# Kernel tuning notes

Measured on AMD Instinct MI355X. Metric: run time of the kernel, lower is better.

## Reference

```python
import jax, jax.numpy as jnp
import numpy as np


def _get_mask(in_features, out_features, in_flow_features, mask_type=None):
    # Faithful port of the torch get_mask() used by MADE.
    if mask_type == 'input':
        in_degrees = np.arange(in_features) % in_flow_features
    else:
        in_degrees = np.arange(in_features) % (in_flow_features - 1)
    if mask_type == 'output':
        out_degrees = np.arange(out_features) % in_flow_features - 1
    else:
        out_degrees = np.arange(out_features) % (in_flow_features - 1)
    return jnp.asarray((out_degrees[:, None] >= in_degrees[None, :]).astype(np.float32))


def setup_inputs() -> dict:
    B, D, H = 8192, 128, 2048
    key = jax.random.key(0)
    ks = jax.random.split(key, 7)
    w_scale_in = 1.0 / np.sqrt(D)
    w_scale_h = 1.0 / np.sqrt(H)
    return {
        'inputs': jax.random.normal(ks[0], (B, D), dtype=jnp.float32),
        's_w0': jax.random.normal(ks[1], (H, D), dtype=jnp.float32) * w_scale_in,
        's_b0': jnp.zeros((H,), dtype=jnp.float32),
        's_w1': jax.random.normal(ks[2], (H, H), dtype=jnp.float32) * w_scale_h,
        's_b1': jnp.zeros((H,), dtype=jnp.float32),
        's_w2': jax.random.normal(ks[3], (D, H), dtype=jnp.float32) * w_scale_h,
        's_b2': jnp.zeros((D,), dtype=jnp.float32),
        't_w0': jax.random.normal(ks[4], (H, D), dtype=jnp.float32) * w_scale_in,
        't_b0': jnp.zeros((H,), dtype=jnp.float32),
        't_w1': jax.random.normal(ks[5], (H, H), dtype=jnp.float32) * w_scale_h,
        't_b1': jnp.zeros((H,), dtype=jnp.float32),
        't_w2': jax.random.normal(ks[6], (D, H), dtype=jnp.float32) * w_scale_h,
        't_b2': jnp.zeros((D,), dtype=jnp.float32),
    }


def reference(inputs, s_w0, s_b0, s_w1, s_b1, s_w2, s_b2,
              t_w0, t_b0, t_w1, t_b1, t_w2, t_b2):
    # MADESplit forward, mode='direct', num_cond_inputs=None, pre_exp_tanh=False.
    D = inputs.shape[1]
    H = s_w0.shape[0]
    m_in = _get_mask(D, H, D, 'input')    # [H, D]
    m_h = _get_mask(H, H, D)              # [H, H]
    m_out = _get_mask(H, D, D, 'output')  # [D, H]

    def masked_mlp(w0, b0, w1, b1, w2, b2, act):
        h = act(inputs @ (m_in * w0).T + b0)   # joiner + first trunk activation
        h = act(h @ (m_h * w1).T + b1)
        return h @ (m_out * w2).T + b2

    m = masked_mlp(s_w0, s_b0, s_w1, s_b1, s_w2, s_b2, jnp.tanh)
    a = masked_mlp(t_w0, t_b0, t_w1, t_b1, t_w2, t_b2, jax.nn.relu)
    u = (inputs - m) * jnp.exp(-a)
    return u, -a.sum(-1, keepdims=True)
```

## Files before the change

kernel.cpp:

```cpp
#include <hip/hip_runtime.h>
#include <hip/hip_bf16.h>

typedef unsigned short u16;
typedef __attribute__((ext_vector_type(8))) short bf16x8;
typedef __attribute__((ext_vector_type(4))) float f32x4;

constexpr int NB = 8192, ND = 128, NH = 2048;

__device__ __forceinline__ u16 f2bf(float x) {
  union { float f; unsigned u; } v; v.f = x;
  unsigned r = v.u + 0x7fffu + ((v.u >> 16) & 1u);
  return (u16)(r >> 16);
}
__device__ __forceinline__ float bf2f(u16 h) {
  union { unsigned u; float f; } v; v.u = ((unsigned)h) << 16; return v.f;
}
__device__ __forceinline__ void store_split(u16* hi, u16* lo, long i, float v) {
  u16 h = f2bf(v);
  hi[i] = h;
  lo[i] = f2bf(v - bf2f(h));
}

__device__ __forceinline__ int deg_sorted(int j) {
  return (j < 272) ? (j / 17) : ((j - 16) >> 4);
}
__device__ __forceinline__ int perm_h(int j) {
  int g, r;
  if (j < 272) { g = j / 17; r = j - g * 17; }
  else         { g = (j - 16) >> 4; r = (j - 16) & 15; }
  return g + 127 * r;
}
__device__ __forceinline__ int offset_of_deg(int g) {
  return (g < 16) ? 17 * g : 16 * g + 16;
}

__device__ __forceinline__ void gll16(const u16* g, u16* l) {
  __builtin_amdgcn_global_load_lds(
      (const __attribute__((address_space(1))) unsigned*)g,
      (__attribute__((address_space(3))) unsigned*)l, 16, 0, 0);
}

__device__ __forceinline__ f32x4 mfma_bb(bf16x8 a, bf16x8 b, f32x4 c) {
  return __builtin_amdgcn_mfma_f32_16x16x32_bf16(a, b, c, 0, 0, 0);
}

template <int PHASE>
__global__ void prep_small(const float* __restrict__ x,
                           const float* __restrict__ w0,
                           const float* __restrict__ b0, const float* __restrict__ b1,
                           u16* __restrict__ xhi, u16* __restrict__ xlo,
                           u16* __restrict__ w0hi, u16* __restrict__ w0lo,
                           float* __restrict__ b0p, float* __restrict__ b1p) {
  constexpr int XB  = (NB * ND) / 256;
  constexpr int W0B = (NH * ND) / 256;
  int bid = blockIdx.x;
  const int tid = threadIdx.x;

  if (PHASE == 0) {
    if (bid < XB) {
      long i = (long)bid * 256 + tid;
      store_split(xhi, xlo, i, x[i]);
      return;
    }
    bid -= XB;
  }
  if (bid < W0B) {
    int i = bid * 256 + tid;
    int r_out = i >> 7, c = i & 127;
    float v = (deg_sorted(r_out) >= c) ? w0[perm_h(r_out) * ND + c] : 0.0f;
    store_split(w0hi, w0lo, i, v);
    return;
  }
  bid -= W0B;
  if (bid < 8) { int j = bid * 256 + tid; b0p[j] = b0[perm_h(j)]; return; }
  { int j = (bid - 8) * 256 + tid; b1p[j] = b1[perm_h(j)]; }
}

__global__ void prep_rows(const float* __restrict__ w1, const float* __restrict__ w2,
                          u16* __restrict__ w1hi, u16* __restrict__ w1lo,
                          u16* __restrict__ w2hi, u16* __restrict__ w2lo) {
  __shared__ float row[NH];
  const int j = blockIdx.x;
  const int tid = threadIdx.x;
  const float* src = (j < NH) ? (w1 + (long)perm_h(j) * NH)
                              : (w2 + (long)(j - NH) * NH);
  const float4* s4 = (const float4*)src;
  float4* r4 = (float4*)row;
#pragma unroll
  for (int i = 0; i < 2; ++i) r4[tid + i * 256] = s4[tid + i * 256];
  __syncthreads();
  if (j < NH) {
    const int dj = deg_sorted(j);
    const long base = (long)j * NH;
#pragma unroll
    for (int k = 0; k < 8; ++k) {
      int c = k * 256 + tid;
      float v = (dj >= deg_sorted(c)) ? row[perm_h(c)] : 0.0f;
      store_split(w1hi, w1lo, base + c, v);
    }
  } else {
    const int r = j - NH;
    const long base = (long)r * NH;
#pragma unroll
    for (int k = 0; k < 8; ++k) {
      int c = k * 256 + tid;
      float v = ((r - 1) >= deg_sorted(c)) ? row[perm_h(c)] : 0.0f;
      store_split(w2hi, w2lo, base + c, v);
    }
  }
}

template <int ACT, int BOUND>
__global__ __launch_bounds__(256, 3) void gemm_split(
    const u16* __restrict__ Ahi, const u16* __restrict__ Alo,
    const u16* __restrict__ Bhi, const u16* __restrict__ Blo,
    const float* __restrict__ bias,
    u16* __restrict__ Chi, u16* __restrict__ Clo,
    float* __restrict__ Cf,
    int M, int N, int K, int ksteps_arg) {
  const int tid = threadIdx.x;
  const int l = tid & 63;
  const int w = tid >> 6;
  const int wr = w >> 1, wc = w & 1;
  const int bm = blockIdx.y * 128;
  const int NT = gridDim.x;
  const int bx = blockIdx.x;
  const int ntile = (bx & 1) ? (bx >> 1) : (NT - 1 - (bx >> 1));
  const int bn = ntile * 128;
  int ksteps;
  if (BOUND == 1) {
    int ghi = deg_sorted(bn + 127);
    ksteps = (ghi + 1 + 31) >> 5;
  } else if (BOUND == 2) {
    int ghi = deg_sorted(bn + 127);
    ksteps = (offset_of_deg(ghi + 1) + 31) >> 5;
  } else {
    ksteps = ksteps_arg;
  }
  const long kbase = (long)blockIdx.z * ksteps * 32;

  __shared__ __align__(16) u16 sAhi[4096];
  __shared__ __align__(16) u16 sAlo[4096];
  __shared__ __align__(16) u16 sBhi[4096];
  __shared__ __align__(16) u16 sBlo[4096];

  f32x4 acc[4][4] = {};

  const int srow = tid >> 2;
  const int scol = (tid & 3) << 3;
  const long aOff0 = (long)(bm + srow) * K + scol + kbase;
  const long aOff1 = aOff0 + 64L * K;
  const long bOff0 = (long)(bn + srow) * K + scol + kbase;
  const long bOff1 = bOff0 + 64L * K;
  const int ldst0 = tid * 8;
  const int ldst1 = 2048 + tid * 8;

  const int fr = l & 15, fq = l >> 4;

  for (int ks = 0; ks < ksteps; ++ks) {
    const long kk = (long)ks * 32;
    __syncthreads();
    gll16(Ahi + aOff0 + kk, sAhi + ldst0);
    gll16(Ahi + aOff1 + kk, sAhi + ldst1);
    gll16(Alo + aOff0 + kk, sAlo + ldst0);
    gll16(Alo + aOff1 + kk, sAlo + ldst1);
    gll16(Bhi + bOff0 + kk, sBhi + ldst0);
    gll16(Bhi + bOff1 + kk, sBhi + ldst1);
    gll16(Blo + bOff0 + kk, sBlo + ldst0);
    gll16(Blo + bOff1 + kk, sBlo + ldst1);
    __syncthreads();

    bf16x8 ah[4], alo[4], bh[4], blo[4];
#pragma unroll
    for (int m = 0; m < 4; ++m) {
      const int off = (wr * 64 + m * 16 + fr) * 32 + fq * 8;
      ah[m]  = *(const bf16x8*)(sAhi + off);
      alo[m] = *(const bf16x8*)(sAlo + off);
    }
#pragma unroll
    for (int n = 0; n < 4; ++n) {
      const int off = (wc * 64 + n * 16 + fr) * 32 + fq * 8;
      bh[n]  = *(const bf16x8*)(sBhi + off);
      blo[n] = *(const bf16x8*)(sBlo + off);
    }
#pragma unroll
    for (int m = 0; m < 4; ++m)
#pragma unroll
      for (int n = 0; n < 4; ++n) {
        acc[m][n] = mfma_bb(ah[m],  bh[n],  acc[m][n]);
        acc[m][n] = mfma_bb(alo[m], bh[n],  acc[m][n]);
        acc[m][n] = mfma_bb(ah[m],  blo[n], acc[m][n]);
      }
  }

  if (ACT == 2) {
    float* out = Cf + (long)blockIdx.z * M * N;
#pragma unroll
    for (int m = 0; m < 4; ++m) {
      const int row = bm + wr * 64 + m * 16 + fq * 4;
#pragma unroll
      for (int n = 0; n < 4; ++n) {
        const int col = bn + wc * 64 + n * 16 + fr;
#pragma unroll
        for (int r = 0; r < 4; ++r)
          out[(long)(row + r) * N + col] = acc[m][n][r];
      }
    }
  } else {
#pragma unroll
    for (int m = 0; m < 4; ++m) {
      const int row = bm + wr * 64 + m * 16 + fq * 4;
#pragma unroll
      for (int n = 0; n < 4; ++n) {
        const int col = bn + wc * 64 + n * 16 + fr;
        const float bv = bias[col];
#pragma unroll
        for (int r = 0; r < 4; ++r) {
          float z = acc[m][n][r] + bv;
          float h = (ACT == 0) ? tanhf(z) : fmaxf(z, 0.0f);
          long idx = (long)(row + r) * N + col;
          store_split(Chi, Clo, idx, h);
        }
      }
    }
  }
}

__global__ void finalize_kernel(const float* __restrict__ x,
                                const float* __restrict__ pm,
                                const float* __restrict__ pa,
                                const float* __restrict__ sb2,
                                const float* __restrict__ tb2,
                                float* __restrict__ out_u,
                                float* __restrict__ out_s) {
  const int b = blockIdx.x * 4 + (threadIdx.x >> 6);
  const int l = threadIdx.x & 63;
  const long base = (long)b * 128;
  float m0 = sb2[l], m1 = sb2[64 + l];
  float a0 = tb2[l], a1 = tb2[64 + l];
#pragma unroll
  for (int k = 0; k < 4; ++k) {
    const long o = (long)k * ((long)NB * ND) + base;
    m0 += pm[o + l];      m1 += pm[o + 64 + l];
    a0 += pa[o + l];      a1 += pa[o + 64 + l];
  }
  out_u[base + l]      = (x[base + l]      - m0) * expf(-a0);
  out_u[base + 64 + l] = (x[base + 64 + l] - m1) * expf(-a1);
  float s = a0 + a1;
#pragma unroll
  for (int off = 32; off; off >>= 1) s += __shfl_down(s, off);
  if (l == 0) out_s[b] = -s;
}

extern "C" void kernel_launch(void* const* d_in, const int* in_sizes, int n_in,
                              void* d_out, int out_size, void* d_ws, size_t ws_size,
                              hipStream_t stream) {
  (void)in_sizes; (void)n_in; (void)out_size; (void)ws_size;
  const float* x   = (const float*)d_in[0];
  const float* sw0 = (const float*)d_in[1];
  const float* sb0 = (const float*)d_in[2];
  const float* sw1 = (const float*)d_in[3];
  const float* sb1 = (const float*)d_in[4];
  const float* sw2 = (const float*)d_in[5];
  const float* sb2 = (const float*)d_in[6];
  const float* tw0 = (const float*)d_in[7];
  const float* tb0 = (const float*)d_in[8];
  const float* tw1 = (const float*)d_in[9];
  const float* tb1 = (const float*)d_in[10];
  const float* tw2 = (const float*)d_in[11];
  const float* tb2 = (const float*)d_in[12];

  char* ws = (char*)d_ws;
  size_t off = 0;
  auto alloc = [&](size_t bytes) {
    void* p = ws + off;
    off += (bytes + 255) & ~(size_t)255;
    return p;
  };
  u16* xhi  = (u16*)alloc((size_t)NB * ND * 2);
  u16* xlo  = (u16*)alloc((size_t)NB * ND * 2);
  u16* w0hi = (u16*)alloc((size_t)NH * ND * 2);
  u16* w0lo = (u16*)alloc((size_t)NH * ND * 2);
  u16* w1hi = (u16*)alloc((size_t)NH * NH * 2);
  u16* w1lo = (u16*)alloc((size_t)NH * NH * 2);
  u16* w2hi = (u16*)alloc((size_t)ND * NH * 2);
  u16* w2lo = (u16*)alloc((size_t)ND * NH * 2);
  u16* h1hi = (u16*)alloc((size_t)NB * NH * 2);
  u16* h1lo = (u16*)alloc((size_t)NB * NH * 2);
  u16* h2hi = (u16*)alloc((size_t)NB * NH * 2);
  u16* h2lo = (u16*)alloc((size_t)NB * NH * 2);
  float* pm  = (float*)alloc((size_t)4 * NB * ND * 4);
  float* pa  = (float*)alloc((size_t)4 * NB * ND * 4);
  float* b0p = (float*)alloc((size_t)NH * 4);
  float* b1p = (float*)alloc((size_t)NH * 4);

  float* out_u = (float*)d_out;
  float* out_s = out_u + (long)NB * ND;

  constexpr int XB   = (NB * ND) / 256;
  constexpr int WSEG = (NH * ND) / 256 + 2 * (NH / 256);

  auto run_mlp = [&](int phase, const float* w0, const float* b0, const float* w1,
                     const float* b1, const float* w2, float* part, bool is_tanh) {
    if (phase == 0)
      prep_small<0><<<XB + WSEG, 256, 0, stream>>>(x, w0, b0, b1, xhi, xlo,
                                                   w0hi, w0lo, b0p, b1p);
    else
      prep_small<1><<<WSEG, 256, 0, stream>>>(x, w0, b0, b1, xhi, xlo,
                                              w0hi, w0lo, b0p, b1p);
    prep_rows<<<NH + ND, 256, 0, stream>>>(w1, w2, w1hi, w1lo, w2hi, w2lo);
    dim3 g12(NH / 128, NB / 128, 1);
    if (is_tanh) {
      gemm_split<0, 1><<<g12, 256, 0, stream>>>(xhi, xlo, w0hi, w0lo, b0p,
                                                h1hi, h1lo, nullptr, NB, NH, ND, 0);
      gemm_split<0, 2><<<g12, 256, 0, stream>>>(h1hi, h1lo, w1hi, w1lo, b1p,
                                                h2hi, h2lo, nullptr, NB, NH, NH, 0);
    } else {
      gemm_split<1, 1><<<g12, 256, 0, stream>>>(xhi, xlo, w0hi, w0lo, b0p,
                                                h1hi, h1lo, nullptr, NB, NH, ND, 0);
      gemm_split<1, 2><<<g12, 256, 0, stream>>>(h1hi, h1lo, w1hi, w1lo, b1p,
                                                h2hi, h2lo, nullptr, NB, NH, NH, 0);
    }
    dim3 g3(1, NB / 128, 4);
    gemm_split<2, 0><<<g3, 256, 0, stream>>>(h2hi, h2lo, w2hi, w2lo, nullptr,
                                             nullptr, nullptr, part, NB, ND, NH,
                                             (NH / 4) / 32);
  };

  run_mlp(0, sw0, sb0, sw1, sb1, sw2, pm, true);
  run_mlp(1, tw0, tb0, tw1, tb1, tw2, pa, false);

  finalize_kernel<<<NB / 4, 256, 0, stream>>>(x, pm, pa, sb2, tb2, out_u, out_s);
}
```

Measured before the change: 601.7 us.

## Replace hidden-layer GEMM with persistent atomic work-queue kernel ordered heaviest-first

The large masked H×H GEMM now runs as a persistent kernel of 1024 blocks that pull 128×128 tiles from a global atomic counter. Tiles are handed out column-tile-major from the heaviest (longest K range) to the lightest, so the unequal triangular work is balanced dynamically and blocks sharing a weight tile run close together for L2 reuse. The first GEMM also drops its interleaved heavy/light tile ordering in favour of a simple reverse order. The scheme adds a counter-init kernel and an atomic plus a barrier per tile, and its single-buffered K loop gives no load/compute overlap.

```diff
diff --git a/kernel.cpp b/kernel.cpp
--- a/kernel.cpp
+++ b/kernel.cpp
@@ -42,6 +42,10 @@
 
 __device__ __forceinline__ f32x4 mfma_bb(bf16x8 a, bf16x8 b, f32x4 c) {
   return __builtin_amdgcn_mfma_f32_16x16x32_bf16(a, b, c, 0, 0, 0);
+}
+
+__global__ void init_ctrs(unsigned* __restrict__ c) {
+  c[threadIdx.x] = 0u;
 }
 
 template <int PHASE>
@@ -106,6 +110,104 @@
       int c = k * 256 + tid;
       float v = ((r - 1) >= deg_sorted(c)) ? row[perm_h(c)] : 0.0f;
       store_split(w2hi, w2lo, base + c, v);
+    }
+  }
+}
+
+template <int ACT>
+__global__ __launch_bounds__(256, 4) void gemm_l2_persist(
+    const u16* __restrict__ Ahi, const u16* __restrict__ Alo,
+    const u16* __restrict__ Bhi, const u16* __restrict__ Blo,
+    const float* __restrict__ bias,
+    u16* __restrict__ Chi, u16* __restrict__ Clo,
+    unsigned* __restrict__ ctr) {
+  constexpr int K = NH;
+  constexpr unsigned NITEMS = (NH / 128) * (NB / 128);
+  const int tid = threadIdx.x;
+  const int l = tid & 63, w = tid >> 6;
+  const int wr = w >> 1, wc = w & 1;
+  const int fr = l & 15, fq = l >> 4;
+
+  __shared__ __align__(16) u16 sAhi[4096];
+  __shared__ __align__(16) u16 sAlo[4096];
+  __shared__ __align__(16) u16 sBhi[4096];
+  __shared__ __align__(16) u16 sBlo[4096];
+  __shared__ unsigned s_item;
+
+  const int srow = tid >> 2;
+  const int scol = (tid & 3) << 3;
+  const int ldst0 = tid * 8;
+  const int ldst1 = 2048 + tid * 8;
+
+  for (;;) {
+    if (tid == 0) s_item = atomicAdd(ctr, 1u);
+    __syncthreads();
+    const unsigned item = s_item;
+    if (item >= NITEMS) break;
+    const int ntile = 15 - (int)(item >> 6);
+    const int bm = (int)(item & 63) * 128;
+    const int bn = ntile * 128;
+    const int ghi = deg_sorted(bn + 127);
+    const int ksteps = (offset_of_deg(ghi + 1) + 31) >> 5;
+
+    const long aOff0 = (long)(bm + srow) * K + scol;
+    const long aOff1 = aOff0 + 64L * K;
+    const long bOff0 = (long)(bn + srow) * K + scol;
+    const long bOff1 = bOff0 + 64L * K;
+
+    f32x4 acc[4][4] = {};
+
+    for (int ks = 0; ks < ksteps; ++ks) {
+      const long kk = (long)ks * 32;
+      __syncthreads();
+      gll16(Ahi + aOff0 + kk, sAhi + ldst0);
+      gll16(Ahi + aOff1 + kk, sAhi + ldst1);
+      gll16(Alo + aOff0 + kk, sAlo + ldst0);
+      gll16(Alo + aOff1 + kk, sAlo + ldst1);
+      gll16(Bhi + bOff0 + kk, sBhi + ldst0);
+      gll16(Bhi + bOff1 + kk, sBhi + ldst1);
+      gll16(Blo + bOff0 + kk, sBlo + ldst0);
+      gll16(Blo + bOff1 + kk, sBlo + ldst1);
+      __syncthreads();
+
+      bf16x8 ah[4], alo[4], bh[4], blo[4];
+#pragma unroll
+      for (int m = 0; m < 4; ++m) {
+        const int off = (wr * 64 + m * 16 + fr) * 32 + fq * 8;
+        ah[m]  = *(const bf16x8*)(sAhi + off);
+        alo[m] = *(const bf16x8*)(sAlo + off);
+      }
+#pragma unroll
+      for (int n = 0; n < 4; ++n) {
+        const int off = (wc * 64 + n * 16 + fr) * 32 + fq * 8;
+        bh[n]  = *(const bf16x8*)(sBhi + off);
+        blo[n] = *(const bf16x8*)(sBlo + off);
+      }
+#pragma unroll
+      for (int m = 0; m < 4; ++m)
+#pragma unroll
+        for (int n = 0; n < 4; ++n) {
+          acc[m][n] = mfma_bb(ah[m],  bh[n],  acc[m][n]);
+          acc[m][n] = mfma_bb(alo[m], bh[n],  acc[m][n]);
+          acc[m][n] = mfma_bb(ah[m],  blo[n], acc[m][n]);
+        }
+    }
+
+#pragma unroll
+    for (int m = 0; m < 4; ++m) {
+      const int row = bm + wr * 64 + m * 16 + fq * 4;
+#pragma unroll
+      for (int n = 0; n < 4; ++n) {
+        const int col = bn + wc * 64 + n * 16 + fr;
+        const float bv = bias[col];
+#pragma unroll
+        for (int r = 0; r < 4; ++r) {
+          float z = acc[m][n][r] + bv;
+          float h = (ACT == 0) ? tanhf(z) : fmaxf(z, 0.0f);
+          long idx = (long)(row + r) * NH + col;
+          store_split(Chi, Clo, idx, h);
+        }
+      }
     }
   }
 }
@@ -123,17 +225,12 @@
   const int w = tid >> 6;
   const int wr = w >> 1, wc = w & 1;
   const int bm = blockIdx.y * 128;
-  const int NT = gridDim.x;
-  const int bx = blockIdx.x;
-  const int ntile = (bx & 1) ? (bx >> 1) : (NT - 1 - (bx >> 1));
+  const int ntile = gridDim.x - 1 - blockIdx.x;
   const int bn = ntile * 128;
   int ksteps;
   if (BOUND == 1) {
     int ghi = deg_sorted(bn + 127);
     ksteps = (ghi + 1 + 31) >> 5;
-  } else if (BOUND == 2) {
-    int ghi = deg_sorted(bn + 127);
-    ksteps = (offset_of_deg(ghi + 1) + 31) >> 5;
   } else {
     ksteps = ksteps_arg;
   }
@@ -289,16 +386,19 @@
   u16* h1lo = (u16*)alloc((size_t)NB * NH * 2);
   u16* h2hi = (u16*)alloc((size_t)NB * NH * 2);
   u16* h2lo = (u16*)alloc((size_t)NB * NH * 2);
-  float* pm  = (float*)alloc((size_t)4 * NB * ND * 4);
-  float* pa  = (float*)alloc((size_t)4 * NB * ND * 4);
-  float* b0p = (float*)alloc((size_t)NH * 4);
-  float* b1p = (float*)alloc((size_t)NH * 4);
+  float* pm   = (float*)alloc((size_t)4 * NB * ND * 4);
+  float* pa   = (float*)alloc((size_t)4 * NB * ND * 4);
+  float* b0p  = (float*)alloc((size_t)NH * 4);
+  float* b1p  = (float*)alloc((size_t)NH * 4);
+  unsigned* ctrs = (unsigned*)alloc(256);
 
   float* out_u = (float*)d_out;
   float* out_s = out_u + (long)NB * ND;
 
   constexpr int XB   = (NB * ND) / 256;
   constexpr int WSEG = (NH * ND) / 256 + 2 * (NH / 256);
+
+  init_ctrs<<<1, 64, 0, stream>>>(ctrs);
 
   auto run_mlp = [&](int phase, const float* w0, const float* b0, const float* w1,
                      const float* b1, const float* w2, float* part, bool is_tanh) {
@@ -309,17 +409,17 @@
       prep_small<1><<<WSEG, 256, 0, stream>>>(x, w0, b0, b1, xhi, xlo,
                                               w0hi, w0lo, b0p, b1p);
     prep_rows<<<NH + ND, 256, 0, stream>>>(w1, w2, w1hi, w1lo, w2hi, w2lo);
-    dim3 g12(NH / 128, NB / 128, 1);
+    dim3 g1(NH / 128, NB / 128, 1);
     if (is_tanh) {
-      gemm_split<0, 1><<<g12, 256, 0, stream>>>(xhi, xlo, w0hi, w0lo, b0p,
-                                                h1hi, h1lo, nullptr, NB, NH, ND, 0);
-      gemm_split<0, 2><<<g12, 256, 0, stream>>>(h1hi, h1lo, w1hi, w1lo, b1p,
-                                                h2hi, h2lo, nullptr, NB, NH, NH, 0);
+      gemm_split<0, 1><<<g1, 256, 0, stream>>>(xhi, xlo, w0hi, w0lo, b0p,
+                                               h1hi, h1lo, nullptr, NB, NH, ND, 0);
+      gemm_l2_persist<0><<<1024, 256, 0, stream>>>(h1hi, h1lo, w1hi, w1lo, b1p,
+                                                   h2hi, h2lo, ctrs + phase * 8);
     } else {
-      gemm_split<1, 1><<<g12, 256, 0, stream>>>(xhi, xlo, w0hi, w0lo, b0p,
-                                                h1hi, h1lo, nullptr, NB, NH, ND, 0);
-      gemm_split<1, 2><<<g12, 256, 0, stream>>>(h1hi, h1lo, w1hi, w1lo, b1p,
-                                                h2hi, h2lo, nullptr, NB, NH, NH, 0);
+      gemm_split<1, 1><<<g1, 256, 0, stream>>>(xhi, xlo, w0hi, w0lo, b0p,
+                                               h1hi, h1lo, nullptr, NB, NH, ND, 0);
+      gemm_l2_persist<1><<<1024, 256, 0, stream>>>(h1hi, h1lo, w1hi, w1lo, b1p,
+                                                   h2hi, h2lo, ctrs + phase * 8);
     }
     dim3 g3(1, NB / 128, 4);
     gemm_split<2, 0><<<g3, 256, 0, stream>>>(h2hi, h2lo, w2hi, w2lo, nullptr,
```

Result: no change. 591.0 us (-1.8%).
